# Kernel optimization log

Hardware: AMD Instinct MI355X
Metric: run time of the kernel (lower is better)

Reference implementation:

```python
import jax, jax.numpy as jnp
import numpy as np

P = 5        # window_size
HEADS = 8
DH = 32      # dim_head
SCALE = DH ** -0.5


def setup_inputs() -> dict:
    key = jax.random.key(0)
    ks = jax.random.split(key, 5)
    b, c, h = 32, 256, 4000
    inner = HEADS * DH  # 256
    x = jax.random.normal(ks[0], (b, c, h), dtype=jnp.float32)
    W_qkv = jax.random.normal(ks[1], (c, inner * 3), dtype=jnp.float32) * (c ** -0.5)
    W_out = jax.random.normal(ks[2], (inner, c), dtype=jnp.float32) * (inner ** -0.5)
    b_out = jax.random.normal(ks[3], (c,), dtype=jnp.float32) * 0.02
    pos_embedding = jax.random.normal(ks[4], (2 * P - 1, 2 * P - 1), dtype=jnp.float32) * 0.02
    return {"x": x, "W_qkv": W_qkv, "W_out": W_out, "b_out": b_out, "pos_embedding": pos_embedding}


def _local_attn(x, W_qkv, W_out, b_out, pos_embedding):
    b, c, h = x.shape
    n = h // P
    # relative-position bias, faithful to torch indexing: rel_index[:,0]=(p-1-a), rel_index[:,1]=(p-a), shape (p,1)
    a = jnp.arange(P)
    bias = pos_embedding[(P - 1 - a)[:, None], (P - a)[:, None]]  # (p, 1)
    mask = jnp.zeros((P, P), x.dtype) + bias                      # (p, p)
    # 'b c (n p) -> (b n) p c'
    xw = x.reshape(b, c, n, P).transpose(0, 2, 3, 1).reshape(b * n, P, c)
    qkv = xw @ W_qkv  # (B, p, 3*inner)
    q, k, v = jnp.split(qkv, 3, axis=-1)
    split_heads = lambda t: t.reshape(b * n, P, HEADS, DH).transpose(0, 2, 1, 3)  # (B, h, p, d)
    q, k, v = split_heads(q), split_heads(k), split_heads(v)
    dots = jnp.einsum('bhid,bhjd->bhij', q, k) * SCALE + mask
    attn = jax.nn.softmax(dots, axis=-1)
    out = jnp.einsum('bhij,bhjd->bhid', attn, v)            # (B, h, p, d)
    out = out.transpose(0, 2, 1, 3).reshape(b * n, P, HEADS * DH)
    out = out @ W_out + b_out                                # (B, p, c_out)
    # '(b n) p c -> b c (n p)'
    out = out.reshape(b, n, P, -1).transpose(0, 3, 1, 2).reshape(b, -1, n * P)
    return out, attn


def reference(x, W_qkv, W_out, b_out, pos_embedding):
    return _local_attn(x, W_qkv, W_out, b_out, pos_embedding)
```

## Files before the change

### kernel.cpp

```cpp
#include <hip/hip_runtime.h>
#include <hip/hip_bf16.h>

typedef __attribute__((ext_vector_type(8))) short short8;
typedef __attribute__((ext_vector_type(4))) float f32x4;

namespace {
constexpr int kC = 256;
constexpr int kH = 4000;
constexpr int kNW = 800;
constexpr int kP = 5;
constexpr float kScale = 0.17677669529663687f;
constexpr int kTotalWin = 25600;

constexpr int WPB = 6;
constexpr int ROWS = WPB * kP;
constexpr int MT = 2;
constexpr int NTHR = 512;

constexpr int WQKV_PACKED = 3 * 16 * 8 * 64 * 8;
constexpr int WOUT_PACKED = 16 * 8 * 64 * 8;

constexpr int RKOFF = 15360;
constexpr int RVT = 30720;
constexpr int SM_TOTAL = 47104;
}

__device__ inline unsigned short f2bs(float f) {
  __hip_bfloat16 h = __float2bfloat16(f);
  return *reinterpret_cast<unsigned short*>(&h);
}

__global__ void prep_weights(const float* __restrict__ Wqkv,
                             const float* __restrict__ Wout,
                             __hip_bfloat16* __restrict__ wq_p,
                             __hip_bfloat16* __restrict__ wo_p) {
  int idx = blockIdx.x * 256 + threadIdx.x;
  if (idx < WQKV_PACKED) {
    int i = idx & 7;
    int l = (idx >> 3) & 63;
    int kt = (idx >> 9) & 7;
    int nt = (idx >> 12) & 15;
    int part = idx >> 16;
    int k = kt * 32 + (l >> 4) * 8 + i;
    int col = part * 256 + nt * 16 + (l & 15);
    wq_p[idx] = __float2bfloat16(Wqkv[k * 768 + col]);
  }
  if (idx < WOUT_PACKED) {
    int i = idx & 7;
    int l = (idx >> 3) & 63;
    int kt = (idx >> 9) & 7;
    int nt = (idx >> 12) & 15;
    int k = kt * 32 + (l >> 4) * 8 + i;
    int col = nt * 16 + (l & 15);
    wo_p[idx] = __float2bfloat16(Wout[k * 256 + col]);
  }
}

__global__ __launch_bounds__(NTHR, 3) void local_attn_kernel(
    const float* __restrict__ x, const short* __restrict__ wq_p,
    const short* __restrict__ wo_p, const float* __restrict__ b_out,
    float* __restrict__ g_out, float* __restrict__ g_attn) {
  __shared__ __align__(16) char smem[SM_TOTAL];

  const int tid = threadIdx.x;
  const int lane = tid & 63;
  const int wid = tid >> 6;

  const int widx0 = blockIdx.x * WPB;
  const int nwin = min(WPB, kTotalWin - widx0);
  const int nrows = nwin * kP;

  for (int i = tid; i < (kC / 2) * ROWS; i += NTHR) {
    int cp = i / ROWS, hh = i % ROWS;
    if (hh < nrows) {
      int gw = widx0 + hh / kP;
      int b = gw / kNW;
      int hl = (gw - b * kNW) * kP + hh % kP;
      const float* p = x + ((size_t)b * kC + 2 * cp) * kH + hl;
      unsigned u = (unsigned)f2bs(p[0]) | ((unsigned)f2bs(p[kH]) << 16);
      *(unsigned*)(smem + hh * 512 + ((cp * 4) ^ ((hh & 7) << 4))) = u;
    }
  }
  for (int i = tid; i < (ROWS - nrows) * 128; i += NTHR)
    *(unsigned*)(smem + (nrows + i / 128) * 512 + (i % 128) * 4) = 0u;
  if (tid < 256) {
    int h = tid >> 5, d = tid & 31;
    int phys = 3 ^ ((d >> 1) & 3);
    *(unsigned*)(smem + RVT + h * 2048 + d * 64 + phys * 16 + 12) = 0u;
  }
  __syncthreads();

  for (int pi = 0; pi < 2; ++pi) {
    const int part = pi + 1;
    f32x4 acc[MT][2];
#pragma unroll
    for (int m = 0; m < MT; ++m)
#pragma unroll
      for (int n = 0; n < 2; ++n) acc[m][n] = (f32x4){0.f, 0.f, 0.f, 0.f};
#pragma unroll
    for (int kt = 0; kt < 8; ++kt) {
      short8 a[MT];
#pragma unroll
      for (int m = 0; m < MT; ++m) {
        int row = m * 16 + (lane & 15);
        int kb = kt * 64 + ((lane >> 4) << 4);
        a[m] = *(const short8*)(smem + row * 512 + (kb ^ ((row & 7) << 4)));
      }
      short8 b[2];
#pragma unroll
      for (int n = 0; n < 2; ++n) {
        int nt = wid * 2 + n;
        b[n] = *(const short8*)(wq_p +
                                ((((part * 16 + nt) * 8 + kt) * 64 + lane) * 8));
      }
#pragma unroll
      for (int m = 0; m < MT; ++m)
#pragma unroll
        for (int n = 0; n < 2; ++n)
          acc[m][n] = __builtin_amdgcn_mfma_f32_16x16x32_bf16(a[m], b[n],
                                                              acc[m][n], 0, 0, 0);
    }
    if (part == 1) {
#pragma unroll
      for (int m = 0; m < MT; ++m)
#pragma unroll
        for (int n = 0; n < 2; ++n)
#pragma unroll
          for (int r = 0; r < 4; ++r) {
            int row = m * 16 + ((lane >> 4) << 2) + r;
            if (row < ROWS) {
              int col = wid * 32 + n * 16 + (lane & 15);
              *(__hip_bfloat16*)(smem + RKOFF + row * 512 +
                                 ((col * 2) ^ ((row & 7) << 4))) =
                  __float2bfloat16(acc[m][n][r]);
            }
          }
    } else {
#pragma unroll
      for (int m = 0; m < MT; ++m)
#pragma unroll
        for (int n = 0; n < 2; ++n)
#pragma unroll
          for (int r = 0; r < 4; ++r) {
            int ks = m * 16 + ((lane >> 4) << 2) + r;
            if (ks < ROWS) {
              int d = n * 16 + (lane & 15);
              int lb = ks * 2;
              int phys = (lb >> 4) ^ ((d >> 1) & 3);
              *(__hip_bfloat16*)(smem + RVT + wid * 2048 + d * 64 + phys * 16 +
                                 (lb & 15)) = __float2bfloat16(acc[m][n][r]);
            }
          }
    }
  }
  {
    f32x4 accq[MT][2];
#pragma unroll
    for (int m = 0; m < MT; ++m)
#pragma unroll
      for (int n = 0; n < 2; ++n) accq[m][n] = (f32x4){0.f, 0.f, 0.f, 0.f};
#pragma unroll
    for (int kt = 0; kt < 8; ++kt) {
      short8 a[MT];
#pragma unroll
      for (int m = 0; m < MT; ++m) {
        int row = m * 16 + (lane & 15);
        int kb = kt * 64 + ((lane >> 4) << 4);
        a[m] = *(const short8*)(smem + row * 512 + (kb ^ ((row & 7) << 4)));
      }
      short8 b[2];
#pragma unroll
      for (int n = 0; n < 2; ++n) {
        int nt = wid * 2 + n;
        b[n] = *(const short8*)(wq_p + (((nt * 8 + kt) * 64 + lane) * 8));
      }
#pragma unroll
      for (int m = 0; m < MT; ++m)
#pragma unroll
        for (int n = 0; n < 2; ++n)
          accq[m][n] = __builtin_amdgcn_mfma_f32_16x16x32_bf16(a[m], b[n],
                                                               accq[m][n], 0, 0, 0);
    }
    __syncthreads();
#pragma unroll
    for (int m = 0; m < MT; ++m)
#pragma unroll
      for (int n = 0; n < 2; ++n)
#pragma unroll
        for (int r = 0; r < 4; ++r) {
          int row = m * 16 + ((lane >> 4) << 2) + r;
          if (row < ROWS) {
            int col = wid * 32 + n * 16 + (lane & 15);
            *(__hip_bfloat16*)(smem + row * 512 + ((col * 2) ^ ((row & 7) << 4))) =
                __float2bfloat16(accq[m][n][r]);
          }
        }
  }
  __syncthreads();

  {
    short8 kfa[2], qfb[2], va[2];
#pragma unroll
    for (int t = 0; t < 2; ++t) {
      int row = t * 16 + (lane & 15);
      int cb = (wid * 64 + ((lane >> 4) << 4)) ^ ((row & 7) << 4);
      kfa[t] = *(const short8*)(smem + RKOFF + row * 512 + cb);
      qfb[t] = *(const short8*)(smem + row * 512 + cb);
      va[t] = *(const short8*)(smem + RVT + wid * 2048 + row * 64 +
                               (((lane >> 4) ^ ((row >> 1) & 3)) << 4));
    }
    f32x4 sacc[2][2];
#pragma unroll
    for (int mk = 0; mk < 2; ++mk)
#pragma unroll
      for (int nq = 0; nq < 2; ++nq) {
        sacc[mk][nq] = __builtin_amdgcn_mfma_f32_16x16x32_bf16(
            kfa[mk], qfb[nq], (f32x4){0.f, 0.f, 0.f, 0.f}, 0, 0, 0);
#pragma unroll
        for (int r = 0; r < 4; ++r) sacc[mk][nq][r] *= kScale;
      }

    const int g = lane >> 4;
    const int alo = ((g & 1) << 1) * 16 + (lane & 15);
    const int ahi = alo + 16;
    const bool ghi = g >= 2;

#pragma unroll
    for (int nq = 0; nq < 2; ++nq) {
      const int q_abs = nq * 16 + (lane & 15);
      float s8[8];
#pragma unroll
      for (int r = 0; r < 4; ++r) {
        float v0l = __shfl(sacc[0][nq][r], alo);
        float v1l = __shfl(sacc[1][nq][r], alo);
        float v0h = __shfl(sacc[0][nq][r], ahi);
        float v1h = __shfl(sacc[1][nq][r], ahi);
        s8[r] = ghi ? v1l : v0l;
        s8[4 + r] = ghi ? v1h : v0h;
      }
      const int w = q_abs / 5;
      const int lo = w * 5;
      float p8[8], psum = 0.f;
#pragma unroll
      for (int i = 0; i < 8; ++i) {
        int kk = g * 8 + i;
        bool in = (q_abs < ROWS) && (kk >= lo) && (kk < lo + 5);
        float e = in ? __expf(s8[i]) : 0.f;
        p8[i] = e;
        psum += e;
      }
      psum += __shfl_xor(psum, 16);
      psum += __shfl_xor(psum, 32);
      float inv = psum > 0.f ? 1.f / psum : 0.f;
      short8 pb;
#pragma unroll
      for (int i = 0; i < 8; ++i) {
        p8[i] *= inv;
        pb[i] = (short)f2bs(p8[i]);
      }
      if (q_abs < nrows) {
        int iq = q_abs - lo;
        float* ap =
            g_attn + (size_t)(widx0 + w) * 200 + wid * 25 + iq * 5 - lo;
#pragma unroll
        for (int i = 0; i < 8; ++i) {
          int kk = g * 8 + i;
          if (kk >= lo && kk < lo + 5) ap[kk] = p8[i];
        }
      }
#pragma unroll
      for (int mt = 0; mt < 2; ++mt) {
        f32x4 o = __builtin_amdgcn_mfma_f32_16x16x32_bf16(
            va[mt], pb, (f32x4){0.f, 0.f, 0.f, 0.f}, 0, 0, 0);
        if (q_abs < ROWS) {
          int qsw = (q_abs & 7) << 4;
#pragma unroll
          for (int r = 0; r < 4; ++r) {
            int d = mt * 16 + g * 4 + r;
            *(__hip_bfloat16*)(smem + q_abs * 512 + ((wid * 64 + d * 2) ^ qsw)) =
                __float2bfloat16(o[r]);
          }
        }
      }
    }
  }
  __syncthreads();

  f32x4 acc2[MT][2];
#pragma unroll
  for (int m = 0; m < MT; ++m)
#pragma unroll
    for (int n = 0; n < 2; ++n) acc2[m][n] = (f32x4){0.f, 0.f, 0.f, 0.f};
#pragma unroll
  for (int kt = 0; kt < 8; ++kt) {
    short8 a[MT];
#pragma unroll
    for (int m = 0; m < MT; ++m) {
      int row = m * 16 + (lane & 15);
      int kb = kt * 64 + ((lane >> 4) << 4);
      a[m] = *(const short8*)(smem + row * 512 + (kb ^ ((row & 7) << 4)));
    }
    short8 b[2];
#pragma unroll
    for (int n = 0; n < 2; ++n) {
      int nt = wid * 2 + n;
      b[n] = *(const short8*)(wo_p + (((nt * 8 + kt) * 64 + lane) * 8));
    }
#pragma unroll
    for (int m = 0; m < MT; ++m)
#pragma unroll
      for (int n = 0; n < 2; ++n)
        acc2[m][n] = __builtin_amdgcn_mfma_f32_16x16x32_bf16(a[m], b[n],
                                                             acc2[m][n], 0, 0, 0);
  }
  float* outS = (float*)(smem + RKOFF);
#pragma unroll
  for (int n = 0; n < 2; ++n) {
    int col = wid * 32 + n * 16 + (lane & 15);
    float bias = b_out[col];
#pragma unroll
    for (int m = 0; m < MT; ++m)
#pragma unroll
      for (int r = 0; r < 4; ++r) {
        int row = m * 16 + ((lane >> 4) << 2) + r;
        if (row < ROWS) outS[col * ROWS + row] = acc2[m][n][r] + bias;
      }
  }
  __syncthreads();

  for (int i = tid; i < kC * ROWS; i += NTHR) {
    int c = i / ROWS, hh = i % ROWS;
    if (hh < nrows) {
      int gw = widx0 + hh / kP;
      int b = gw / kNW;
      int hl = (gw - b * kNW) * kP + hh % kP;
      g_out[((size_t)b * kC + c) * kH + hl] = outS[c * ROWS + hh];
    }
  }
}

extern "C" void kernel_launch(void* const* d_in, const int* in_sizes, int n_in,
                              void* d_out, int out_size, void* d_ws,
                              size_t ws_size, hipStream_t stream) {
  const float* x = (const float*)d_in[0];
  const float* Wqkv = (const float*)d_in[1];
  const float* Wout = (const float*)d_in[2];
  const float* bout = (const float*)d_in[3];

  short* wq_p = (short*)d_ws;
  short* wo_p = wq_p + WQKV_PACKED;

  prep_weights<<<WQKV_PACKED / 256, 256, 0, stream>>>(
      Wqkv, Wout, (__hip_bfloat16*)wq_p, (__hip_bfloat16*)wo_p);

  float* g_out = (float*)d_out;
  float* g_attn = g_out + (size_t)32 * kC * kH;

  int nblocks = (kTotalWin + WPB - 1) / WPB;
  local_attn_kernel<<<nblocks, NTHR, 0, stream>>>(x, wq_p, wo_p, bout, g_out,
                                                  g_attn);
}
```

Measured before the change: 194.1 us.

## Keep V and softmax probabilities in registers and store output directly from MFMA results

The V projection result now stays in registers and feeds a 16x16x16 bf16 MFMA directly. The score accumulators are softmaxed in place without cross-lane shuffles, which removes the transposed V shared buffer and cuts LDS from 47 KB to 32 KB, raising possible occupancy. The final output no longer stages through shared memory with an extra barrier. Blocks whose windows all lie in one batch write float2 vectors straight from the accumulators to global memory, and other blocks use a scalar fallback. The input load is also restructured into a fixed unrolled loop that writes zeros for padding rows.

```diff
diff --git a/kernel.cpp b/kernel.cpp
--- a/kernel.cpp
+++ b/kernel.cpp
@@ -2,7 +2,9 @@
 #include <hip/hip_bf16.h>
 
 typedef __attribute__((ext_vector_type(8))) short short8;
+typedef __attribute__((ext_vector_type(4))) short short4v;
 typedef __attribute__((ext_vector_type(4))) float f32x4;
+typedef __attribute__((ext_vector_type(2))) float f32x2;
 
 namespace {
 constexpr int kC = 256;
@@ -14,20 +16,32 @@
 
 constexpr int WPB = 6;
 constexpr int ROWS = WPB * kP;
-constexpr int MT = 2;
 constexpr int NTHR = 512;
 
 constexpr int WQKV_PACKED = 3 * 16 * 8 * 64 * 8;
 constexpr int WOUT_PACKED = 16 * 8 * 64 * 8;
 
-constexpr int RKOFF = 15360;
-constexpr int RVT = 30720;
-constexpr int SM_TOTAL = 47104;
+constexpr int RKOFF = 16384;
+constexpr int SM_TOTAL = 32768;
 }
 
 __device__ inline unsigned short f2bs(float f) {
   __hip_bfloat16 h = __float2bfloat16(f);
   return *reinterpret_cast<unsigned short*>(&h);
+}
+
+__device__ inline f32x4 mfma16(short4v a, short4v b, f32x4 c) {
+#if __has_builtin(__builtin_amdgcn_mfma_f32_16x16x16bf16_1k)
+  return __builtin_amdgcn_mfma_f32_16x16x16bf16_1k(a, b, c, 0, 0, 0);
+#elif __has_builtin(__builtin_amdgcn_mfma_f32_16x16x16_bf16)
+  return __builtin_amdgcn_mfma_f32_16x16x16_bf16(a, b, c, 0, 0, 0);
+#else
+  f32x4 d;
+  asm("v_mfma_f32_16x16x16_bf16 %0, %1, %2, %3"
+      : "=v"(d)
+      : "v"(a), "v"(b), "v"(c));
+  return d;
+#endif
 }
 
 __global__ void prep_weights(const float* __restrict__ Wqkv,
@@ -65,133 +79,131 @@
   const int tid = threadIdx.x;
   const int lane = tid & 63;
   const int wid = tid >> 6;
+  const int g = lane >> 4;
+  const int l15 = lane & 15;
 
   const int widx0 = blockIdx.x * WPB;
   const int nwin = min(WPB, kTotalWin - widx0);
   const int nrows = nwin * kP;
 
-  for (int i = tid; i < (kC / 2) * ROWS; i += NTHR) {
-    int cp = i / ROWS, hh = i % ROWS;
+#pragma unroll
+  for (int pass = 0; pass < 8; ++pass) {
+    int idx = pass * NTHR + tid;
+    int cp = idx >> 5, hh = idx & 31;
+    unsigned u = 0u;
     if (hh < nrows) {
-      int gw = widx0 + hh / kP;
-      int b = gw / kNW;
-      int hl = (gw - b * kNW) * kP + hh % kP;
-      const float* p = x + ((size_t)b * kC + 2 * cp) * kH + hl;
-      unsigned u = (unsigned)f2bs(p[0]) | ((unsigned)f2bs(p[kH]) << 16);
-      *(unsigned*)(smem + hh * 512 + ((cp * 4) ^ ((hh & 7) << 4))) = u;
-    }
-  }
-  for (int i = tid; i < (ROWS - nrows) * 128; i += NTHR)
-    *(unsigned*)(smem + (nrows + i / 128) * 512 + (i % 128) * 4) = 0u;
-  if (tid < 256) {
-    int h = tid >> 5, d = tid & 31;
-    int phys = 3 ^ ((d >> 1) & 3);
-    *(unsigned*)(smem + RVT + h * 2048 + d * 64 + phys * 16 + 12) = 0u;
+      int wl = hh / kP, il = hh - wl * kP;
+      int gw = widx0 + wl;
+      int bb = gw / kNW;
+      int hl = (gw - bb * kNW) * kP + il;
+      const float* p = x + ((size_t)bb * kC + 2 * cp) * kH + hl;
+      u = (unsigned)f2bs(p[0]) | ((unsigned)f2bs(p[kH]) << 16);
+    }
+    *(unsigned*)(smem + hh * 512 + ((cp * 4) ^ ((hh & 7) << 4))) = u;
   }
   __syncthreads();
 
-  for (int pi = 0; pi < 2; ++pi) {
-    const int part = pi + 1;
-    f32x4 acc[MT][2];
-#pragma unroll
-    for (int m = 0; m < MT; ++m)
+  f32x4 acc_v[2][2];
+  {
+    f32x4 acc[2][2];
+#pragma unroll
+    for (int m = 0; m < 2; ++m)
 #pragma unroll
       for (int n = 0; n < 2; ++n) acc[m][n] = (f32x4){0.f, 0.f, 0.f, 0.f};
 #pragma unroll
     for (int kt = 0; kt < 8; ++kt) {
-      short8 a[MT];
-#pragma unroll
-      for (int m = 0; m < MT; ++m) {
-        int row = m * 16 + (lane & 15);
-        int kb = kt * 64 + ((lane >> 4) << 4);
+      short8 a[2];
+#pragma unroll
+      for (int m = 0; m < 2; ++m) {
+        int row = m * 16 + l15;
+        int kb = kt * 64 + (g << 4);
         a[m] = *(const short8*)(smem + row * 512 + (kb ^ ((row & 7) << 4)));
       }
-      short8 b[2];
 #pragma unroll
       for (int n = 0; n < 2; ++n) {
-        int nt = wid * 2 + n;
-        b[n] = *(const short8*)(wq_p +
-                                ((((part * 16 + nt) * 8 + kt) * 64 + lane) * 8));
-      }
-#pragma unroll
-      for (int m = 0; m < MT; ++m)
-#pragma unroll
-        for (int n = 0; n < 2; ++n)
-          acc[m][n] = __builtin_amdgcn_mfma_f32_16x16x32_bf16(a[m], b[n],
-                                                              acc[m][n], 0, 0, 0);
-    }
-    if (part == 1) {
-#pragma unroll
-      for (int m = 0; m < MT; ++m)
-#pragma unroll
-        for (int n = 0; n < 2; ++n)
-#pragma unroll
-          for (int r = 0; r < 4; ++r) {
-            int row = m * 16 + ((lane >> 4) << 2) + r;
-            if (row < ROWS) {
-              int col = wid * 32 + n * 16 + (lane & 15);
-              *(__hip_bfloat16*)(smem + RKOFF + row * 512 +
-                                 ((col * 2) ^ ((row & 7) << 4))) =
-                  __float2bfloat16(acc[m][n][r]);
-            }
-          }
-    } else {
-#pragma unroll
-      for (int m = 0; m < MT; ++m)
-#pragma unroll
-        for (int n = 0; n < 2; ++n)
-#pragma unroll
-          for (int r = 0; r < 4; ++r) {
-            int ks = m * 16 + ((lane >> 4) << 2) + r;
-            if (ks < ROWS) {
-              int d = n * 16 + (lane & 15);
-              int lb = ks * 2;
-              int phys = (lb >> 4) ^ ((d >> 1) & 3);
-              *(__hip_bfloat16*)(smem + RVT + wid * 2048 + d * 64 + phys * 16 +
-                                 (lb & 15)) = __float2bfloat16(acc[m][n][r]);
-            }
-          }
+        short8 b = *(const short8*)(
+            wq_p + ((((16 + wid * 2 + n) * 8 + kt) * 64 + lane) * 8));
+#pragma unroll
+        for (int m = 0; m < 2; ++m)
+          acc[m][n] =
+              __builtin_amdgcn_mfma_f32_16x16x32_bf16(a[m], b, acc[m][n], 0, 0, 0);
+      }
+    }
+#pragma unroll
+    for (int m = 0; m < 2; ++m)
+#pragma unroll
+      for (int n = 0; n < 2; ++n)
+#pragma unroll
+        for (int r = 0; r < 4; ++r) {
+          int row = m * 16 + (g << 2) + r;
+          if (row < ROWS) {
+            int col = wid * 32 + n * 16 + l15;
+            *(__hip_bfloat16*)(smem + RKOFF + row * 512 +
+                               ((col * 2) ^ ((row & 7) << 4))) =
+                __float2bfloat16(acc[m][n][r]);
+          }
+        }
+#pragma unroll
+    for (int m = 0; m < 2; ++m)
+#pragma unroll
+      for (int n = 0; n < 2; ++n) acc_v[m][n] = (f32x4){0.f, 0.f, 0.f, 0.f};
+#pragma unroll
+    for (int kt = 0; kt < 8; ++kt) {
+      short8 a[2];
+#pragma unroll
+      for (int m = 0; m < 2; ++m) {
+        int row = m * 16 + l15;
+        int kb = kt * 64 + (g << 4);
+        a[m] = *(const short8*)(smem + row * 512 + (kb ^ ((row & 7) << 4)));
+      }
+#pragma unroll
+      for (int n = 0; n < 2; ++n) {
+        short8 b = *(const short8*)(
+            wq_p + ((((32 + wid * 2 + n) * 8 + kt) * 64 + lane) * 8));
+#pragma unroll
+        for (int m = 0; m < 2; ++m)
+          acc_v[m][n] = __builtin_amdgcn_mfma_f32_16x16x32_bf16(a[m], b,
+                                                                acc_v[m][n], 0, 0, 0);
+      }
     }
   }
   {
-    f32x4 accq[MT][2];
-#pragma unroll
-    for (int m = 0; m < MT; ++m)
+    f32x4 accq[2][2];
+#pragma unroll
+    for (int m = 0; m < 2; ++m)
 #pragma unroll
       for (int n = 0; n < 2; ++n) accq[m][n] = (f32x4){0.f, 0.f, 0.f, 0.f};
 #pragma unroll
     for (int kt = 0; kt < 8; ++kt) {
-      short8 a[MT];
-#pragma unroll
-      for (int m = 0; m < MT; ++m) {
-        int row = m * 16 + (lane & 15);
-        int kb = kt * 64 + ((lane >> 4) << 4);
+      short8 a[2];
+#pragma unroll
+      for (int m = 0; m < 2; ++m) {
+        int row = m * 16 + l15;
+        int kb = kt * 64 + (g << 4);
         a[m] = *(const short8*)(smem + row * 512 + (kb ^ ((row & 7) << 4)));
       }
-      short8 b[2];
 #pragma unroll
       for (int n = 0; n < 2; ++n) {
-        int nt = wid * 2 + n;
-        b[n] = *(const short8*)(wq_p + (((nt * 8 + kt) * 64 + lane) * 8));
-      }
-#pragma unroll
-      for (int m = 0; m < MT; ++m)
-#pragma unroll
-        for (int n = 0; n < 2; ++n)
-          accq[m][n] = __builtin_amdgcn_mfma_f32_16x16x32_bf16(a[m], b[n],
-                                                               accq[m][n], 0, 0, 0);
+        short8 b = *(const short8*)(
+            wq_p + ((((wid * 2 + n) * 8 + kt) * 64 + lane) * 8));
+#pragma unroll
+        for (int m = 0; m < 2; ++m)
+          accq[m][n] =
+              __builtin_amdgcn_mfma_f32_16x16x32_bf16(a[m], b, accq[m][n], 0, 0, 0);
+      }
     }
     __syncthreads();
 #pragma unroll
-    for (int m = 0; m < MT; ++m)
+    for (int m = 0; m < 2; ++m)
 #pragma unroll
       for (int n = 0; n < 2; ++n)
 #pragma unroll
         for (int r = 0; r < 4; ++r) {
-          int row = m * 16 + ((lane >> 4) << 2) + r;
+          int row = m * 16 + (g << 2) + r;
           if (row < ROWS) {
-            int col = wid * 32 + n * 16 + (lane & 15);
-            *(__hip_bfloat16*)(smem + row * 512 + ((col * 2) ^ ((row & 7) << 4))) =
+            int col = wid * 32 + n * 16 + l15;
+            *(__hip_bfloat16*)(smem + row * 512 +
+                               ((col * 2) ^ ((row & 7) << 4))) =
                 __float2bfloat16(accq[m][n][r]);
           }
         }
@@ -199,142 +211,151 @@
   __syncthreads();
 
   {
-    short8 kfa[2], qfb[2], va[2];
+    short8 kfa[2], qfb[2];
+    const int cb = wid * 64 + (g << 4);
 #pragma unroll
     for (int t = 0; t < 2; ++t) {
-      int row = t * 16 + (lane & 15);
-      int cb = (wid * 64 + ((lane >> 4) << 4)) ^ ((row & 7) << 4);
-      kfa[t] = *(const short8*)(smem + RKOFF + row * 512 + cb);
-      qfb[t] = *(const short8*)(smem + row * 512 + cb);
-      va[t] = *(const short8*)(smem + RVT + wid * 2048 + row * 64 +
-                               (((lane >> 4) ^ ((row >> 1) & 3)) << 4));
+      int row = t * 16 + l15;
+      int sw = (row & 7) << 4;
+      kfa[t] = *(const short8*)(smem + RKOFF + row * 512 + (cb ^ sw));
+      qfb[t] = *(const short8*)(smem + row * 512 + (cb ^ sw));
     }
     f32x4 sacc[2][2];
 #pragma unroll
     for (int mk = 0; mk < 2; ++mk)
 #pragma unroll
-      for (int nq = 0; nq < 2; ++nq) {
+      for (int nq = 0; nq < 2; ++nq)
         sacc[mk][nq] = __builtin_amdgcn_mfma_f32_16x16x32_bf16(
             kfa[mk], qfb[nq], (f32x4){0.f, 0.f, 0.f, 0.f}, 0, 0, 0);
-#pragma unroll
-        for (int r = 0; r < 4; ++r) sacc[mk][nq][r] *= kScale;
-      }
-
-    const int g = lane >> 4;
-    const int alo = ((g & 1) << 1) * 16 + (lane & 15);
-    const int ahi = alo + 16;
-    const bool ghi = g >= 2;
-
+
+    short4v pb[2][2];
 #pragma unroll
     for (int nq = 0; nq < 2; ++nq) {
-      const int q_abs = nq * 16 + (lane & 15);
-      float s8[8];
-#pragma unroll
-      for (int r = 0; r < 4; ++r) {
-        float v0l = __shfl(sacc[0][nq][r], alo);
-        float v1l = __shfl(sacc[1][nq][r], alo);
-        float v0h = __shfl(sacc[0][nq][r], ahi);
-        float v1h = __shfl(sacc[1][nq][r], ahi);
-        s8[r] = ghi ? v1l : v0l;
-        s8[4 + r] = ghi ? v1h : v0h;
-      }
-      const int w = q_abs / 5;
-      const int lo = w * 5;
-      float p8[8], psum = 0.f;
-#pragma unroll
-      for (int i = 0; i < 8; ++i) {
-        int kk = g * 8 + i;
-        bool in = (q_abs < ROWS) && (kk >= lo) && (kk < lo + 5);
-        float e = in ? __expf(s8[i]) : 0.f;
-        p8[i] = e;
-        psum += e;
-      }
+      int q_abs = nq * 16 + l15;
+      int w = q_abs / kP;
+      int lo = w * kP;
+      float psum = 0.f;
+#pragma unroll
+      for (int mk = 0; mk < 2; ++mk)
+#pragma unroll
+        for (int r = 0; r < 4; ++r) {
+          int k = mk * 16 + (g << 2) + r;
+          bool in = (q_abs < ROWS) && (k >= lo) && (k < lo + kP);
+          float e = in ? __expf(sacc[mk][nq][r] * kScale) : 0.f;
+          sacc[mk][nq][r] = e;
+          psum += e;
+        }
       psum += __shfl_xor(psum, 16);
       psum += __shfl_xor(psum, 32);
       float inv = psum > 0.f ? 1.f / psum : 0.f;
-      short8 pb;
-#pragma unroll
-      for (int i = 0; i < 8; ++i) {
-        p8[i] *= inv;
-        pb[i] = (short)f2bs(p8[i]);
+#pragma unroll
+      for (int mk = 0; mk < 2; ++mk) {
+        short4v t4;
+#pragma unroll
+        for (int r = 0; r < 4; ++r) {
+          float pv = sacc[mk][nq][r] * inv;
+          sacc[mk][nq][r] = pv;
+          t4[r] = (short)f2bs(pv);
+        }
+        pb[mk][nq] = t4;
       }
       if (q_abs < nrows) {
-        int iq = q_abs - lo;
-        float* ap =
-            g_attn + (size_t)(widx0 + w) * 200 + wid * 25 + iq * 5 - lo;
-#pragma unroll
-        for (int i = 0; i < 8; ++i) {
-          int kk = g * 8 + i;
-          if (kk >= lo && kk < lo + 5) ap[kk] = p8[i];
-        }
-      }
+        float* ap = g_attn + (size_t)(widx0 + w) * 200 + wid * 25 +
+                    (q_abs - lo) * 5 - lo;
+#pragma unroll
+        for (int mk = 0; mk < 2; ++mk)
+#pragma unroll
+          for (int r = 0; r < 4; ++r) {
+            int k = mk * 16 + (g << 2) + r;
+            if (k >= lo && k < lo + kP) ap[k] = sacc[mk][nq][r];
+          }
+      }
+    }
+    short4v av[2][2];
+#pragma unroll
+    for (int kb2 = 0; kb2 < 2; ++kb2)
 #pragma unroll
       for (int mt = 0; mt < 2; ++mt) {
-        f32x4 o = __builtin_amdgcn_mfma_f32_16x16x32_bf16(
-            va[mt], pb, (f32x4){0.f, 0.f, 0.f, 0.f}, 0, 0, 0);
+        short4v t4;
+#pragma unroll
+        for (int r = 0; r < 4; ++r) t4[r] = (short)f2bs(acc_v[kb2][mt][r]);
+        av[kb2][mt] = t4;
+      }
+#pragma unroll
+    for (int mt = 0; mt < 2; ++mt)
+#pragma unroll
+      for (int nq = 0; nq < 2; ++nq) {
+        f32x4 o = mfma16(av[0][mt], pb[0][nq], (f32x4){0.f, 0.f, 0.f, 0.f});
+        o = mfma16(av[1][mt], pb[1][nq], o);
+        int q_abs = nq * 16 + l15;
         if (q_abs < ROWS) {
-          int qsw = (q_abs & 7) << 4;
+          short4v o4;
+#pragma unroll
+          for (int r = 0; r < 4; ++r) o4[r] = (short)f2bs(o[r]);
+          int byte = (wid * 64 + mt * 32 + g * 8) ^ ((q_abs & 7) << 4);
+          *(short4v*)(smem + q_abs * 512 + byte) = o4;
+        }
+      }
+  }
+  __syncthreads();
+
+  f32x4 acc2[2][2];
+#pragma unroll
+  for (int m = 0; m < 2; ++m)
+#pragma unroll
+    for (int n = 0; n < 2; ++n) acc2[m][n] = (f32x4){0.f, 0.f, 0.f, 0.f};
+#pragma unroll
+  for (int kt = 0; kt < 8; ++kt) {
+    short8 a[2];
+#pragma unroll
+    for (int m = 0; m < 2; ++m) {
+      int row = m * 16 + l15;
+      int kb = kt * 64 + (g << 4);
+      a[m] = *(const short8*)(smem + row * 512 + (kb ^ ((row & 7) << 4)));
+    }
+#pragma unroll
+    for (int n = 0; n < 2; ++n) {
+      short8 b =
+          *(const short8*)(wo_p + ((((wid * 2 + n) * 8 + kt) * 64 + lane) * 8));
+#pragma unroll
+      for (int m = 0; m < 2; ++m)
+        acc2[m][n] =
+            __builtin_amdgcn_mfma_f32_16x16x32_bf16(a[m], b, acc2[m][n], 0, 0, 0);
+    }
+  }
+  {
+    const int b0 = widx0 / kNW;
+    const bool fast = (nrows == ROWS) && (b0 == (widx0 + WPB - 1) / kNW);
+#pragma unroll
+    for (int n = 0; n < 2; ++n) {
+      int col = wid * 32 + n * 16 + l15;
+      float bias = b_out[col];
+      if (fast) {
+        int h0 = (widx0 - b0 * kNW) * kP;
+        float* op = g_out + ((size_t)b0 * kC + col) * kH + h0 + g * 4;
+#pragma unroll
+        for (int m = 0; m < 2; ++m) {
+          f32x2 v01 = {acc2[m][n][0] + bias, acc2[m][n][1] + bias};
+          *(f32x2*)(op + m * 16) = v01;
+          if (m * 16 + (g << 2) + 2 < ROWS) {
+            f32x2 v23 = {acc2[m][n][2] + bias, acc2[m][n][3] + bias};
+            *(f32x2*)(op + m * 16 + 2) = v23;
+          }
+        }
+      } else {
+#pragma unroll
+        for (int m = 0; m < 2; ++m)
 #pragma unroll
           for (int r = 0; r < 4; ++r) {
-            int d = mt * 16 + g * 4 + r;
-            *(__hip_bfloat16*)(smem + q_abs * 512 + ((wid * 64 + d * 2) ^ qsw)) =
-                __float2bfloat16(o[r]);
-          }
-        }
-      }
-    }
-  }
-  __syncthreads();
-
-  f32x4 acc2[MT][2];
-#pragma unroll
-  for (int m = 0; m < MT; ++m)
-#pragma unroll
-    for (int n = 0; n < 2; ++n) acc2[m][n] = (f32x4){0.f, 0.f, 0.f, 0.f};
-#pragma unroll
-  for (int kt = 0; kt < 8; ++kt) {
-    short8 a[MT];
-#pragma unroll
-    for (int m = 0; m < MT; ++m) {
-      int row = m * 16 + (lane & 15);
-      int kb = kt * 64 + ((lane >> 4) << 4);
-      a[m] = *(const short8*)(smem + row * 512 + (kb ^ ((row & 7) << 4)));
-    }
-    short8 b[2];
-#pragma unroll
-    for (int n = 0; n < 2; ++n) {
-      int nt = wid * 2 + n;
-      b[n] = *(const short8*)(wo_p + (((nt * 8 + kt) * 64 + lane) * 8));
-    }
-#pragma unroll
-    for (int m = 0; m < MT; ++m)
-#pragma unroll
-      for (int n = 0; n < 2; ++n)
-        acc2[m][n] = __builtin_amdgcn_mfma_f32_16x16x32_bf16(a[m], b[n],
-                                                             acc2[m][n], 0, 0, 0);
-  }
-  float* outS = (float*)(smem + RKOFF);
-#pragma unroll
-  for (int n = 0; n < 2; ++n) {
-    int col = wid * 32 + n * 16 + (lane & 15);
-    float bias = b_out[col];
-#pragma unroll
-    for (int m = 0; m < MT; ++m)
-#pragma unroll
-      for (int r = 0; r < 4; ++r) {
-        int row = m * 16 + ((lane >> 4) << 2) + r;
-        if (row < ROWS) outS[col * ROWS + row] = acc2[m][n][r] + bias;
-      }
-  }
-  __syncthreads();
-
-  for (int i = tid; i < kC * ROWS; i += NTHR) {
-    int c = i / ROWS, hh = i % ROWS;
-    if (hh < nrows) {
-      int gw = widx0 + hh / kP;
-      int b = gw / kNW;
-      int hl = (gw - b * kNW) * kP + hh % kP;
-      g_out[((size_t)b * kC + c) * kH + hl] = outS[c * ROWS + hh];
+            int row = m * 16 + (g << 2) + r;
+            if (row < nrows) {
+              int gw = widx0 + row / kP;
+              int bb = gw / kNW;
+              int hl = (gw - bb * kNW) * kP + row % kP;
+              g_out[((size_t)bb * kC + col) * kH + hl] = acc2[m][n][r] + bias;
+            }
+          }
+      }
     }
   }
 }
```

Measured after the change: 202.9 us. +4.5%, slower.
